# Kernel optimization log

Hardware: AMD Instinct MI355X
Metric: run time of the kernel (lower is better)

## Reference

```python
import jax, jax.numpy as jnp
import numpy as np

B, T, C = 8, 16, 2048
H, HD = 16, 128            # head_dim = C // H
MAX_LEN = 4096             # context_len / kv buffer length
CACHE_LEN = 2048           # tokens already in cache
THETA = 10000.0


def _rope_tables(dim, max_len, theta=THETA):
    freqs = 1.0 / theta ** (jnp.arange(0, dim, 2, dtype=jnp.float32) / dim)
    t = jnp.arange(max_len, dtype=jnp.float32)
    f = jnp.outer(t, freqs)                      # [max_len, dim/2]
    return jnp.cos(f), jnp.sin(f)


def _rotate(x):
    # interleaved rotate-half: (x0,x1,x2,x3,...) -> (-x1,x0,-x3,x2,...)
    x1, x2 = x[..., ::2], x[..., 1::2]
    return jnp.stack((-x2, x1), axis=-1).reshape(x.shape)


def setup_inputs() -> dict:
    key = jax.random.key(0)
    ks = jax.random.split(key, 5)
    x = jax.random.normal(ks[0], (B, T, C), dtype=jnp.float32)
    k_buf = jax.random.normal(ks[1], (B, H, MAX_LEN, HD), dtype=jnp.float32)
    v_buf = jax.random.normal(ks[2], (B, H, MAX_LEN, HD), dtype=jnp.float32)
    W_qkv = jax.random.normal(ks[3], (C, 3 * C), dtype=jnp.float32) / np.sqrt(C)
    W_out = jax.random.normal(ks[4], (C, C), dtype=jnp.float32) / np.sqrt(C)
    cos_tab, sin_tab = _rope_tables(HD, MAX_LEN)
    return {"x": x, "k_buf": k_buf, "v_buf": v_buf, "W_qkv": W_qkv,
            "W_out": W_out, "cos_tab": cos_tab, "sin_tab": sin_tab,
            "cache_len": CACHE_LEN}


def reference(x, k_buf, v_buf, W_qkv, W_out, cos_tab, sin_tab, cache_len):
    B_, T_, C_ = x.shape
    H_ = k_buf.shape[1]
    HD_ = C_ // H_
    # fused QKV projection
    qkv = x @ W_qkv                              # [B,T,3C]
    q, k, v = jnp.split(qkv, 3, axis=-1)
    q = q.reshape(B_, T_, H_, HD_).transpose(0, 2, 1, 3)   # [B,H,T,hd]
    k = k.reshape(B_, T_, H_, HD_).transpose(0, 2, 1, 3)
    v = v.reshape(B_, T_, H_, HD_).transpose(0, 2, 1, 3)
    # RoPE at positions [cache_len, cache_len+T)
    cos2 = jnp.repeat(cos_tab[cache_len:cache_len + T_], 2, axis=-1)[None, None]
    sin2 = jnp.repeat(sin_tab[cache_len:cache_len + T_], 2, axis=-1)[None, None]
    q = q * cos2 + _rotate(q) * sin2
    k = k * cos2 + _rotate(k) * sin2
    # KV-cache update (functional)
    k_buf = k_buf.at[:, :, cache_len:cache_len + T_].set(k)
    v_buf = v_buf.at[:, :, cache_len:cache_len + T_].set(v)
    new_len = cache_len + T_
    # masked full-cache attention
    scale = HD_ ** -0.5
    attn = jnp.einsum('bhqd,bhkd->bhqk', q * scale, k_buf)  # [B,H,T,MAX_LEN]
    q_pos = cache_len + jnp.arange(T_)
    k_pos = jnp.arange(k_buf.shape[2])
    mask = (k_pos[None, :] <= q_pos[:, None]) & (k_pos[None, :] < new_len)
    attn = jnp.where(mask[None, None], attn, jnp.finfo(attn.dtype).min)
    out = jnp.einsum('bhqk,bhkd->bhqd', jax.nn.softmax(attn, axis=-1), v_buf)
    out = out.transpose(0, 2, 1, 3).reshape(B_, T_, C_)
    return out @ W_out, k_buf, v_buf
```

## Files before the change

kernel.cpp:

```cpp
#include <hip/hip_runtime.h>

typedef unsigned short u16;
typedef unsigned int   u32;
typedef u16  u16x4 __attribute__((ext_vector_type(4)));
typedef u16  u16x8 __attribute__((ext_vector_type(8)));
typedef u32  u32x4 __attribute__((ext_vector_type(4)));
typedef short s16x8 __attribute__((ext_vector_type(8)));
typedef float f32x2 __attribute__((ext_vector_type(2)));
typedef float f32x4 __attribute__((ext_vector_type(4)));

#define DEVFN static __device__ __forceinline__

DEVFN float bf2f(u16 v) { u32 t = (u32)v << 16; return __builtin_bit_cast(float, t); }
DEVFN u16 f2bf(float f) {
  u32 u = __builtin_bit_cast(u32, f);
  return (u16)((u + 0x7fffu + ((u >> 16) & 1u)) >> 16);
}
DEVFN void unpk(u32 w, float& lo, float& hi) {
  lo = __builtin_bit_cast(float, w << 16);
  hi = __builtin_bit_cast(float, w & 0xffff0000u);
}

constexpr int Bb = 8, Tt = 16, Cc = 2048, Hh = 16, HD = 128, ML = 4096;
constexpr int N3 = 3 * Cc;
constexpr float SCALE = 0.08838834764831845f;
constexpr size_t NKV = (size_t)Bb * Hh * ML * HD;
constexpr int NCH = 6;

constexpr size_t WS_FLAG = 0;
constexpr size_t WS_QKV  = 16;
constexpr size_t WS_PART = 16;
constexpr size_t WS_QBF  = 786448;
constexpr size_t WS_ATTN = 917520;
constexpr size_t WS_TOTAL = 1179664;

DEVFN int san_cl(int raw) {
  if (raw >= 0 && raw <= ML - Tt) return raw;
  float f = __builtin_bit_cast(float, raw);
  int v = (int)f;
  if (v >= 0 && v <= ML - Tt) return v;
  return 0;
}

DEVFN int w12_probe1(const u32* p, long long base, long long stride, int lane) {
  u32 w = p[base + (long long)lane * stride];
  u32 e = (w >> 7) & 0xffu;
  unsigned long long b = __ballot(e >= 100u && e <= 140u);
  return (__popcll(b) >= 32) ? 0 : 1;
}

__global__ void w12_det(const u32* x, const u32* kb, const u32* vb,
                        const u32* wq, const u32* wo, const u32* ct,
                        const u32* st, int* flags)
{
  int lane = threadIdx.x;
  int f0 = w12_probe1(x,  40000,    997,    lane);
  int f1 = w12_probe1(kb, 10000000, 300001, lane);
  int f2 = w12_probe1(vb, 10000000, 300001, lane);
  int f3 = w12_probe1(wq, 2000000,  33331,  lane);
  int f4 = w12_probe1(wo, 700000,   17177,  lane);
  int f5 = w12_probe1(ct, 40000,    997,    lane);
  int f6 = w12_probe1(st, 40000,    997,    lane);
  if (lane == 0) {
    flags[0] = f0; flags[1] = f1; flags[2] = f2; flags[3] = f3;
    flags[4] = f4; flags[5] = f5; flags[6] = f6; flags[7] = 0;
  }
}

DEVFN void w12_mm_core(const void* __restrict__ A, const void* __restrict__ W,
                       int ldn, int fa, int fw, int kbeg, int m0, int n0,
                       u16 (&As)[64][72], u16 (&Bs)[8][66][8], f32x4 (&acc)[4])
{
  const int tid = threadIdx.x;
  const int l = tid & 63, wv = tid >> 6;
  for (int k0 = kbeg; k0 < kbeg + 512; k0 += 64) {
    __syncthreads();
#pragma unroll
    for (int it = 0; it < 2; ++it) {
      int idx = it * 256 + tid, row = idx >> 3, kc = (idx & 7) * 8;
      if (fa) {
        const float* Af = (const float*)A + (size_t)(m0 + row) * Cc + k0 + kc;
        f32x4 a0 = *(const f32x4*)Af;
        f32x4 a1 = *(const f32x4*)(Af + 4);
        u16x8 av;
#pragma unroll
        for (int u = 0; u < 4; ++u) { av[u] = f2bf(a0[u]); av[u + 4] = f2bf(a1[u]); }
        *(u16x8*)&As[row][kc] = av;
      } else {
        u16x8 av = *(const u16x8*)((const u16*)A + (size_t)(m0 + row) * Cc + k0 + kc);
        *(u16x8*)&As[row][kc] = av;
      }
    }
#pragma unroll
    for (int i = 0; i < 4; ++i) {
      int kk = i * 16 + (tid >> 4);
      int nn = (tid & 15) * 4;
      if (fw) {
        f32x4 bv = *(const f32x4*)((const float*)W + (size_t)(k0 + kk) * ldn + n0 + nn);
#pragma unroll
        for (int u = 0; u < 4; ++u) Bs[kk >> 3][nn + u][kk & 7] = f2bf(bv[u]);
      } else {
        u16x4 bv = *(const u16x4*)((const u16*)W + (size_t)(k0 + kk) * ldn + n0 + nn);
#pragma unroll
        for (int u = 0; u < 4; ++u) Bs[kk >> 3][nn + u][kk & 7] = bv[u];
      }
    }
    __syncthreads();
#pragma unroll
    for (int ks = 0; ks < 2; ++ks) {
      s16x8 a = __builtin_bit_cast(s16x8,
          *(const u16x8*)&As[wv * 16 + (l & 15)][ks * 32 + (l >> 4) * 8]);
#pragma unroll
      for (int nf = 0; nf < 4; ++nf) {
        s16x8 b = __builtin_bit_cast(s16x8,
            *(const u16x8*)&Bs[ks * 4 + (l >> 4)][nf * 16 + (l & 15)][0]);
        acc[nf] = __builtin_amdgcn_mfma_f32_16x16x32_bf16(a, b, acc[nf], 0, 0, 0);
      }
    }
  }
}

__global__ __launch_bounds__(256) void w12_mmp(const void* __restrict__ A,
    const void* __restrict__ W, int ldn, float* __restrict__ part,
    const int* __restrict__ flags)
{
  __shared__ u16 As[64][72];
  __shared__ u16 Bs[8][66][8];
  const int n0 = blockIdx.x * 64, m0 = blockIdx.y * 64, s = blockIdx.z;
  f32x4 acc[4] = {{0.f,0.f,0.f,0.f},{0.f,0.f,0.f,0.f},
                  {0.f,0.f,0.f,0.f},{0.f,0.f,0.f,0.f}};
  w12_mm_core(A, W, ldn, flags[0], flags[3], s * 512, m0, n0, As, Bs, acc);
  const int l = threadIdx.x & 63, wv = threadIdx.x >> 6;
  const int row = m0 + wv * 16 + (l >> 4) * 4;
  const int colb = n0 + (l & 15);
  float* pb = part + (size_t)s * 128 * ldn;
#pragma unroll
  for (int nf = 0; nf < 4; ++nf)
#pragma unroll
    for (int j = 0; j < 4; ++j)
      pb[(size_t)(row + j) * ldn + colb + nf * 16] = acc[nf][j];
}

__global__ __launch_bounds__(256) void w12_red1(const float* __restrict__ part,
                                                float* __restrict__ qkv)
{
  size_t e4 = (size_t)blockIdx.x * 256 + threadIdx.x;
  f32x4 acc = {0.f, 0.f, 0.f, 0.f};
#pragma unroll
  for (int s = 0; s < 4; ++s) {
    f32x4 v = *(const f32x4*)&part[(size_t)s * 786432 + e4 * 4];
    acc[0] += v[0]; acc[1] += v[1]; acc[2] += v[2]; acc[3] += v[3];
  }
  *(f32x4*)&qkv[e4 * 4] = acc;
}

__global__ __launch_bounds__(256) void w12_mma(const float* __restrict__ A,
    const void* __restrict__ W, int ldn, float* __restrict__ outp,
    const int* __restrict__ flags)
{
  __shared__ u16 As[64][72];
  __shared__ u16 Bs[8][66][8];
  const int n0 = blockIdx.x * 64, m0 = blockIdx.y * 64, s = blockIdx.z;
  f32x4 acc[4] = {{0.f,0.f,0.f,0.f},{0.f,0.f,0.f,0.f},
                  {0.f,0.f,0.f,0.f},{0.f,0.f,0.f,0.f}};
  w12_mm_core(A, W, ldn, 1, flags[4], s * 512, m0, n0, As, Bs, acc);
  const int l = threadIdx.x & 63, wv = threadIdx.x >> 6;
  const int row = m0 + wv * 16 + (l >> 4) * 4;
  const int colb = n0 + (l & 15);
#pragma unroll
  for (int nf = 0; nf < 4; ++nf)
#pragma unroll
    for (int j = 0; j < 4; ++j)
      atomicAdd(&outp[(size_t)(row + j) * ldn + colb + nf * 16], acc[nf][j]);
}

__global__ __launch_bounds__(256) void w12_zero(float* __restrict__ outp) {
  size_t i = ((size_t)blockIdx.x * 256 + threadIdx.x) * 4;
  f32x4 z = {0.f, 0.f, 0.f, 0.f};
  *(f32x4*)&outp[i] = z;
}

__global__ __launch_bounds__(256) void w12_rot(const float* __restrict__ qkv,
    const void* __restrict__ ct, const void* __restrict__ st,
    const int* __restrict__ clp, u16* __restrict__ qbf,
    float* __restrict__ outk, float* __restrict__ outv,
    const int* __restrict__ flags)
{
  const int m = blockIdx.x, b = m >> 4, t = m & 15;
  const int half = blockIdx.y;
  const int cl = san_cl(*clp), pos = cl + t;
  const int fc = flags[5], fs = flags[6];
  const float* qr = qkv + (size_t)m * N3;
  for (int i0 = half * 512 + threadIdx.x; i0 < half * 512 + 512; i0 += 256) {
    int h = i0 >> 6, i = i0 & 63;
    float cs = fc ? ((const float*)ct)[pos * 64 + i] : bf2f(((const u16*)ct)[pos * 64 + i]);
    float sn = fs ? ((const float*)st)[pos * 64 + i] : bf2f(((const u16*)st)[pos * 64 + i]);
    int col = h * HD + 2 * i;
    float q0 = qr[col], q1 = qr[col + 1];
    qbf[(size_t)m * Cc + col]     = f2bf((q0 * cs - q1 * sn) * SCALE);
    qbf[(size_t)m * Cc + col + 1] = f2bf((q1 * cs + q0 * sn) * SCALE);
    float k0 = qr[2048 + col], k1 = qr[2048 + col + 1];
    size_t ko = ((size_t)(b * Hh + h) * ML + pos) * HD + 2 * i;
    outk[ko]     = k0 * cs - k1 * sn;
    outk[ko + 1] = k1 * cs + k0 * sn;
    outv[ko]     = qr[4096 + col];
    outv[ko + 1] = qr[4096 + col + 1];
  }
}

__global__ __launch_bounds__(256) void w12_attc(
    const void* __restrict__ kin, const void* __restrict__ vin,
    const u16* __restrict__ qbf, const int* __restrict__ clp,
    float* __restrict__ outk, float* __restrict__ outv,
    float* __restrict__ part, float* __restrict__ mlb,
    const int* __restrict__ flags)
{
  __shared__ u32 kls[64][68];
  __shared__ u32 vls[64][68];
  __shared__ u32 qls[16][68];
  __shared__ float pls[16][68];

  const int tid = threadIdx.x;
  const int chunk = blockIdx.x;
  const int bh = blockIdx.y;
  const int cl = san_cl(*clp), nl = cl + Tt;
  const int fk = flags[1], fv = flags[2];
  const size_t base = (size_t)bh * ML * HD;
  const int b = bh >> 4, h = bh & 15;

  {
    const u16* qsrc = qbf + (size_t)b * Tt * Cc + h * HD;
    int r = tid >> 4, c8 = tid & 15;
    u16x8 qv = *(const u16x8*)&qsrc[(size_t)r * Cc + c8 * 8];
    *(u32x4*)&qls[r][c8 * 4] = __builtin_bit_cast(u32x4, qv);
  }

  const int t = tid >> 4;
  const int js = tid & 15;
  const int qpos = cl + t;
  float m_run = -1e30f, l_run = 0.f;
  float O[8] = {0.f,0.f,0.f,0.f,0.f,0.f,0.f,0.f};

  for (int st8 = chunk; st8 < 64; st8 += NCH) {
    const int r0 = st8 * 64;
    __syncthreads();
#pragma unroll
    for (int ii = 0; ii < 4; ++ii) {
      int idx = ii * 256 + tid, r = idx >> 4, c8 = idx & 15;
      int jg = r0 + r;
      size_t off = base + (size_t)jg * HD + c8 * 8;
      bool fresh = (jg >= cl) && (jg < nl);
      f32x4 ka, kb, va, vb;
      if (fresh) {
        ka = *(const f32x4*)&outk[off];
        kb = *(const f32x4*)&outk[off + 4];
        va = *(const f32x4*)&outv[off];
        vb = *(const f32x4*)&outv[off + 4];
      } else {
        if (fk) {
          ka = *(const f32x4*)((const float*)kin + off);
          kb = *(const f32x4*)((const float*)kin + off + 4);
        } else {
          u16x8 kv8 = *(const u16x8*)((const u16*)kin + off);
          for (int u = 0; u < 4; ++u) { ka[u] = bf2f(kv8[u]); kb[u] = bf2f(kv8[u + 4]); }
        }
        if (fv) {
          va = *(const f32x4*)((const float*)vin + off);
          vb = *(const f32x4*)((const float*)vin + off + 4);
        } else {
          u16x8 vv8 = *(const u16x8*)((const u16*)vin + off);
          for (int u = 0; u < 4; ++u) { va[u] = bf2f(vv8[u]); vb[u] = bf2f(vv8[u + 4]); }
        }
        *(f32x4*)&outk[off] = ka;
        *(f32x4*)&outk[off + 4] = kb;
        *(f32x4*)&outv[off] = va;
        *(f32x4*)&outv[off + 4] = vb;
      }
      u16x8 kv, vv;
#pragma unroll
      for (int u = 0; u < 4; ++u) {
        kv[u] = f2bf(ka[u]); kv[u + 4] = f2bf(kb[u]);
        vv[u] = f2bf(va[u]); vv[u + 4] = f2bf(vb[u]);
      }
      *(u32x4*)&kls[r][c8 * 4] = __builtin_bit_cast(u32x4, kv);
      *(u32x4*)&vls[r][c8 * 4] = __builtin_bit_cast(u32x4, vv);
    }
    __syncthreads();
    if (r0 >= nl) continue;

    float s[4] = {0.f,0.f,0.f,0.f};
#pragma unroll
    for (int dblk = 0; dblk < 4; ++dblk) {
      u32x4 qv[4];
#pragma unroll
      for (int g = 0; g < 4; ++g)
        qv[g] = *(const u32x4*)&qls[t][dblk * 16 + g * 4];
      float qf[32];
#pragma unroll
      for (int g = 0; g < 4; ++g)
#pragma unroll
        for (int u = 0; u < 4; ++u)
          unpk(qv[g][u], qf[g * 8 + 2 * u], qf[g * 8 + 2 * u + 1]);
#pragma unroll
      for (int jj = 0; jj < 4; ++jj) {
        const int j = js + jj * 16;
        u32x4 kv4[4];
#pragma unroll
        for (int g = 0; g < 4; ++g)
          kv4[g] = *(const u32x4*)&kls[j][dblk * 16 + g * 4];
        float a_ = s[jj];
#pragma unroll
        for (int g = 0; g < 4; ++g)
#pragma unroll
          for (int u = 0; u < 4; ++u) {
            float lo, hi; unpk(kv4[g][u], lo, hi);
            a_ += qf[g * 8 + 2 * u] * lo;
            a_ += qf[g * 8 + 2 * u + 1] * hi;
          }
        s[jj] = a_;
      }
    }

    float mt = -1e30f;
    bool val[4];
#pragma unroll
    for (int jj = 0; jj < 4; ++jj) {
      int jg = r0 + js + jj * 16;
      val[jj] = (jg <= qpos);
      if (!val[jj]) s[jj] = -1e30f;
      mt = fmaxf(mt, s[jj]);
    }
#pragma unroll
    for (int w = 1; w < 16; w <<= 1)
      mt = fmaxf(mt, __shfl_xor(mt, w));
    float mn = fmaxf(m_run, mt);
    float crr = __expf(m_run - mn);
    float p[4], ps = 0.f;
#pragma unroll
    for (int jj = 0; jj < 4; ++jj) {
      p[jj] = val[jj] ? __expf(s[jj] - mn) : 0.f;
      ps += p[jj];
    }
#pragma unroll
    for (int w = 1; w < 16; w <<= 1)
      ps += __shfl_xor(ps, w);
    l_run = l_run * crr + ps;
    m_run = mn;
#pragma unroll
    for (int jj = 0; jj < 4; ++jj)
      pls[t][js + jj * 16] = p[jj];
#pragma unroll
    for (int e = 0; e < 8; ++e) O[e] *= crr;
    __syncthreads();

    const int jmax = (nl - r0 < 64) ? (nl - r0) : 64;
#pragma unroll 2
    for (int j = 0; j < jmax; ++j) {
      float pv = pls[t][j];
      u32x4 vw = *(const u32x4*)&vls[j][js * 4];
#pragma unroll
      for (int g = 0; g < 4; ++g) {
        float lo, hi; unpk(vw[g], lo, hi);
        O[2 * g]     += pv * lo;
        O[2 * g + 1] += pv * hi;
      }
    }
  }

  const int slot = bh * NCH + chunk;
  u16* ob = (u16*)(part + (size_t)slot * 1024);
  u16x8 ov;
#pragma unroll
  for (int e = 0; e < 8; ++e) ov[e] = f2bf(O[e]);
  *(u16x8*)&ob[t * HD + js * 8] = ov;
  if (js == 0) { mlb[slot * 32 + t] = m_run; mlb[slot * 32 + 16 + t] = l_run; }
}

__global__ __launch_bounds__(128) void w12_comb(const float* __restrict__ part,
    const float* __restrict__ mlb, float* __restrict__ attn)
{
  const int row = blockIdx.x;
  const int d = threadIdx.x;
  const int bh = row >> 4, t = row & 15;
  float M = -1e30f;
#pragma unroll
  for (int c = 0; c < NCH; ++c) M = fmaxf(M, mlb[(bh * NCH + c) * 32 + t]);
  float L = 0.f, acc = 0.f;
#pragma unroll
  for (int c = 0; c < NCH; ++c) {
    const int slot = bh * NCH + c;
    float w = __expf(mlb[slot * 32 + t] - M);
    L   += w * mlb[slot * 32 + 16 + t];
    acc += w * bf2f(((const u16*)(part + (size_t)slot * 1024))[t * HD + d]);
  }
  const int b = bh >> 4, h = bh & 15;
  attn[(size_t)(b * Tt + t) * Cc + h * HD + d] = acc / L;
}

extern "C" void kernel_launch(void* const* d_in, const int* in_sizes, int n_in,
                              void* d_out, int out_size, void* d_ws, size_t ws_size,
                              hipStream_t stream)
{
  const void* x    = d_in[0];
  const void* kin  = d_in[1];
  const void* vin  = d_in[2];
  const void* wqkv = d_in[3];
  const void* wout = d_in[4];
  const void* ct   = d_in[5];
  const void* st   = d_in[6];
  const int*  clp  = (const int*)d_in[7];

  float* out_f = (float*)d_out;
  float* outk  = out_f + (size_t)Bb * Tt * Cc;
  float* outv  = outk + NKV;
  float* ws = (float*)d_ws;

  if (ws_size < WS_TOTAL * sizeof(float)) return;

  int* flags = (int*)(ws + WS_FLAG);
  u16* qbf   = (u16*)(ws + WS_QBF);

  w12_det<<<1, 64, 0, stream>>>((const u32*)x, (const u32*)kin, (const u32*)vin,
                                (const u32*)wqkv, (const u32*)wout,
                                (const u32*)ct, (const u32*)st, flags);
  w12_mmp<<<dim3(N3 / 64, 2, 4), 256, 0, stream>>>(x, wqkv, N3, outv, flags);
  w12_red1<<<768, 256, 0, stream>>>(outv, ws + WS_QKV);
  w12_rot<<<dim3(128, 2), 256, 0, stream>>>(ws + WS_QKV, ct, st, clp, qbf,
                                            outk, outv, flags);
  w12_attc<<<dim3(NCH, 128), 256, 0, stream>>>(kin, vin, qbf, clp, outk, outv,
                                               ws + WS_PART, out_f, flags);
  w12_comb<<<2048, 128, 0, stream>>>(ws + WS_PART, out_f, ws + WS_ATTN);
  w12_zero<<<256, 256, 0, stream>>>(out_f);
  w12_mma<<<dim3(Cc / 64, 2, 4), 256, 0, stream>>>(ws + WS_ATTN, wout, Cc,
                                                   out_f, flags);
}
```

Measured before the change: 303.6 us.

## Prefetch next KV tile into registers while computing attention on current tile

The attention kernel now software-pipelines its KV tile loop. It loads the next tile's K/V rows into registers before computing scores and the PV product on the current shared-memory tile, and it drops one barrier per iteration. Tiles beyond the valid length are handled in a separate copy-only loop that only copies the cache to the output. Launch bounds now request 3 blocks per CU. The cost is more register pressure from the prefetch buffers, which may spill or cut occupancy.

```diff
diff --git a/kernel.cpp b/kernel.cpp
--- a/kernel.cpp
+++ b/kernel.cpp
@@ -42,32 +42,32 @@
   return 0;
 }
 
-DEVFN int w12_probe1(const u32* p, long long base, long long stride, int lane) {
+DEVFN int w13_probe1(const u32* p, long long base, long long stride, int lane) {
   u32 w = p[base + (long long)lane * stride];
   u32 e = (w >> 7) & 0xffu;
   unsigned long long b = __ballot(e >= 100u && e <= 140u);
   return (__popcll(b) >= 32) ? 0 : 1;
 }
 
-__global__ void w12_det(const u32* x, const u32* kb, const u32* vb,
+__global__ void w13_det(const u32* x, const u32* kb, const u32* vb,
                         const u32* wq, const u32* wo, const u32* ct,
                         const u32* st, int* flags)
 {
   int lane = threadIdx.x;
-  int f0 = w12_probe1(x,  40000,    997,    lane);
-  int f1 = w12_probe1(kb, 10000000, 300001, lane);
-  int f2 = w12_probe1(vb, 10000000, 300001, lane);
-  int f3 = w12_probe1(wq, 2000000,  33331,  lane);
-  int f4 = w12_probe1(wo, 700000,   17177,  lane);
-  int f5 = w12_probe1(ct, 40000,    997,    lane);
-  int f6 = w12_probe1(st, 40000,    997,    lane);
+  int f0 = w13_probe1(x,  40000,    997,    lane);
+  int f1 = w13_probe1(kb, 10000000, 300001, lane);
+  int f2 = w13_probe1(vb, 10000000, 300001, lane);
+  int f3 = w13_probe1(wq, 2000000,  33331,  lane);
+  int f4 = w13_probe1(wo, 700000,   17177,  lane);
+  int f5 = w13_probe1(ct, 40000,    997,    lane);
+  int f6 = w13_probe1(st, 40000,    997,    lane);
   if (lane == 0) {
     flags[0] = f0; flags[1] = f1; flags[2] = f2; flags[3] = f3;
     flags[4] = f4; flags[5] = f5; flags[6] = f6; flags[7] = 0;
   }
 }
 
-DEVFN void w12_mm_core(const void* __restrict__ A, const void* __restrict__ W,
+DEVFN void w13_mm_core(const void* __restrict__ A, const void* __restrict__ W,
                        int ldn, int fa, int fw, int kbeg, int m0, int n0,
                        u16 (&As)[64][72], u16 (&Bs)[8][66][8], f32x4 (&acc)[4])
 {
@@ -120,7 +120,7 @@
   }
 }
 
-__global__ __launch_bounds__(256) void w12_mmp(const void* __restrict__ A,
+__global__ __launch_bounds__(256) void w13_mmp(const void* __restrict__ A,
     const void* __restrict__ W, int ldn, float* __restrict__ part,
     const int* __restrict__ flags)
 {
@@ -129,7 +129,7 @@
   const int n0 = blockIdx.x * 64, m0 = blockIdx.y * 64, s = blockIdx.z;
   f32x4 acc[4] = {{0.f,0.f,0.f,0.f},{0.f,0.f,0.f,0.f},
                   {0.f,0.f,0.f,0.f},{0.f,0.f,0.f,0.f}};
-  w12_mm_core(A, W, ldn, flags[0], flags[3], s * 512, m0, n0, As, Bs, acc);
+  w13_mm_core(A, W, ldn, flags[0], flags[3], s * 512, m0, n0, As, Bs, acc);
   const int l = threadIdx.x & 63, wv = threadIdx.x >> 6;
   const int row = m0 + wv * 16 + (l >> 4) * 4;
   const int colb = n0 + (l & 15);
@@ -141,7 +141,7 @@
       pb[(size_t)(row + j) * ldn + colb + nf * 16] = acc[nf][j];
 }
 
-__global__ __launch_bounds__(256) void w12_red1(const float* __restrict__ part,
+__global__ __launch_bounds__(256) void w13_red1(const float* __restrict__ part,
                                                 float* __restrict__ qkv)
 {
   size_t e4 = (size_t)blockIdx.x * 256 + threadIdx.x;
@@ -154,7 +154,7 @@
   *(f32x4*)&qkv[e4 * 4] = acc;
 }
 
-__global__ __launch_bounds__(256) void w12_mma(const float* __restrict__ A,
+__global__ __launch_bounds__(256) void w13_mma(const float* __restrict__ A,
     const void* __restrict__ W, int ldn, float* __restrict__ outp,
     const int* __restrict__ flags)
 {
@@ -163,7 +163,7 @@
   const int n0 = blockIdx.x * 64, m0 = blockIdx.y * 64, s = blockIdx.z;
   f32x4 acc[4] = {{0.f,0.f,0.f,0.f},{0.f,0.f,0.f,0.f},
                   {0.f,0.f,0.f,0.f},{0.f,0.f,0.f,0.f}};
-  w12_mm_core(A, W, ldn, 1, flags[4], s * 512, m0, n0, As, Bs, acc);
+  w13_mm_core(A, W, ldn, 1, flags[4], s * 512, m0, n0, As, Bs, acc);
   const int l = threadIdx.x & 63, wv = threadIdx.x >> 6;
   const int row = m0 + wv * 16 + (l >> 4) * 4;
   const int colb = n0 + (l & 15);
@@ -174,13 +174,13 @@
       atomicAdd(&outp[(size_t)(row + j) * ldn + colb + nf * 16], acc[nf][j]);
 }
 
-__global__ __launch_bounds__(256) void w12_zero(float* __restrict__ outp) {
+__global__ __launch_bounds__(256) void w13_zero(float* __restrict__ outp) {
   size_t i = ((size_t)blockIdx.x * 256 + threadIdx.x) * 4;
   f32x4 z = {0.f, 0.f, 0.f, 0.f};
   *(f32x4*)&outp[i] = z;
 }
 
-__global__ __launch_bounds__(256) void w12_rot(const float* __restrict__ qkv,
+__global__ __launch_bounds__(256) void w13_rot(const float* __restrict__ qkv,
     const void* __restrict__ ct, const void* __restrict__ st,
     const int* __restrict__ clp, u16* __restrict__ qbf,
     float* __restrict__ outk, float* __restrict__ outv,
@@ -208,7 +208,72 @@
   }
 }
 
-__global__ __launch_bounds__(256) void w12_attc(
+DEVFN void w13_bkunpk(u32x4 w, f32x4& a, f32x4& b) {
+  a[0] = bf2f((u16)(w[0] & 0xffffu)); a[1] = bf2f((u16)(w[0] >> 16));
+  a[2] = bf2f((u16)(w[1] & 0xffffu)); a[3] = bf2f((u16)(w[1] >> 16));
+  b[0] = bf2f((u16)(w[2] & 0xffffu)); b[1] = bf2f((u16)(w[2] >> 16));
+  b[2] = bf2f((u16)(w[3] & 0xffffu)); b[3] = bf2f((u16)(w[3] >> 16));
+}
+
+DEVFN void w13_load_tile(const void* kin, const void* vin,
+    const float* outk, const float* outv, size_t base, int r0, int rr, int c8,
+    int cl, int nl, int fk, int fv,
+    f32x4 (&RK)[8], f32x4 (&RV)[8], u32x4 (&BK)[4], u32x4 (&BV)[4])
+{
+#pragma unroll
+  for (int ii = 0; ii < 4; ++ii) {
+    int jg = r0 + ii * 16 + rr;
+    size_t off = base + (size_t)jg * HD + c8 * 8;
+    bool fr = (jg >= cl) && (jg < nl);
+    if (fr) {
+      RK[2*ii] = *(const f32x4*)&outk[off]; RK[2*ii+1] = *(const f32x4*)&outk[off+4];
+      RV[2*ii] = *(const f32x4*)&outv[off]; RV[2*ii+1] = *(const f32x4*)&outv[off+4];
+    } else {
+      if (fk) {
+        RK[2*ii]   = *(const f32x4*)((const float*)kin + off);
+        RK[2*ii+1] = *(const f32x4*)((const float*)kin + off + 4);
+      } else BK[ii] = *(const u32x4*)((const u16*)kin + off);
+      if (fv) {
+        RV[2*ii]   = *(const f32x4*)((const float*)vin + off);
+        RV[2*ii+1] = *(const f32x4*)((const float*)vin + off + 4);
+      } else BV[ii] = *(const u32x4*)((const u16*)vin + off);
+    }
+  }
+}
+
+DEVFN void w13_write_tile(float* outk, float* outv, size_t base, int r0,
+    int rr, int c8, int cl, int nl, int fk, int fv,
+    const f32x4 (&RK)[8], const f32x4 (&RV)[8],
+    const u32x4 (&BK)[4], const u32x4 (&BV)[4],
+    u32 (&kls)[64][68], u32 (&vls)[64][68])
+{
+#pragma unroll
+  for (int ii = 0; ii < 4; ++ii) {
+    int jg = r0 + ii * 16 + rr;
+    int r = ii * 16 + rr;
+    size_t off = base + (size_t)jg * HD + c8 * 8;
+    bool fr = (jg >= cl) && (jg < nl);
+    f32x4 ka, kb, va, vb;
+    if (fr || fk) { ka = RK[2*ii]; kb = RK[2*ii+1]; }
+    else w13_bkunpk(BK[ii], ka, kb);
+    if (fr || fv) { va = RV[2*ii]; vb = RV[2*ii+1]; }
+    else w13_bkunpk(BV[ii], va, vb);
+    if (!fr) {
+      *(f32x4*)&outk[off] = ka; *(f32x4*)&outk[off + 4] = kb;
+      *(f32x4*)&outv[off] = va; *(f32x4*)&outv[off + 4] = vb;
+    }
+    u16x8 kv, vv;
+#pragma unroll
+    for (int u = 0; u < 4; ++u) {
+      kv[u] = f2bf(ka[u]); kv[u + 4] = f2bf(kb[u]);
+      vv[u] = f2bf(va[u]); vv[u + 4] = f2bf(vb[u]);
+    }
+    *(u32x4*)&kls[r][c8 * 4] = __builtin_bit_cast(u32x4, kv);
+    *(u32x4*)&vls[r][c8 * 4] = __builtin_bit_cast(u32x4, vv);
+  }
+}
+
+__global__ __launch_bounds__(256, 3) void w13_attc(
     const void* __restrict__ kin, const void* __restrict__ vin,
     const u16* __restrict__ qbf, const int* __restrict__ clp,
     float* __restrict__ outk, float* __restrict__ outv,
@@ -230,140 +295,137 @@
 
   {
     const u16* qsrc = qbf + (size_t)b * Tt * Cc + h * HD;
-    int r = tid >> 4, c8 = tid & 15;
-    u16x8 qv = *(const u16x8*)&qsrc[(size_t)r * Cc + c8 * 8];
-    *(u32x4*)&qls[r][c8 * 4] = __builtin_bit_cast(u32x4, qv);
+    int r = tid >> 4, c8q = tid & 15;
+    u16x8 qv = *(const u16x8*)&qsrc[(size_t)r * Cc + c8q * 8];
+    *(u32x4*)&qls[r][c8q * 4] = __builtin_bit_cast(u32x4, qv);
   }
 
   const int t = tid >> 4;
   const int js = tid & 15;
+  const int rr = tid >> 4;
+  const int c8 = tid & 15;
   const int qpos = cl + t;
   float m_run = -1e30f, l_run = 0.f;
   float O[8] = {0.f,0.f,0.f,0.f,0.f,0.f,0.f,0.f};
 
-  for (int st8 = chunk; st8 < 64; st8 += NCH) {
+  f32x4 RK[8], RV[8];
+  u32x4 BK[4], BV[4];
+
+  int st8 = chunk;
+  if (st8 * 64 < nl) {
+    w13_load_tile(kin, vin, outk, outv, base, st8 * 64, rr, c8, cl, nl, fk, fv,
+                  RK, RV, BK, BV);
+    while (true) {
+      const int r0 = st8 * 64;
+      __syncthreads();
+      w13_write_tile(outk, outv, base, r0, rr, c8, cl, nl, fk, fv,
+                     RK, RV, BK, BV, kls, vls);
+      __syncthreads();
+      const int nxt = st8 + NCH;
+      const bool more = (nxt * 64 < nl);
+      if (more)
+        w13_load_tile(kin, vin, outk, outv, base, nxt * 64, rr, c8, cl, nl,
+                      fk, fv, RK, RV, BK, BV);
+
+      float s[4] = {0.f,0.f,0.f,0.f};
+#pragma unroll
+      for (int dblk = 0; dblk < 4; ++dblk) {
+        u32x4 qv[4];
+#pragma unroll
+        for (int g = 0; g < 4; ++g)
+          qv[g] = *(const u32x4*)&qls[t][dblk * 16 + g * 4];
+        float qf[32];
+#pragma unroll
+        for (int g = 0; g < 4; ++g)
+#pragma unroll
+          for (int u = 0; u < 4; ++u)
+            unpk(qv[g][u], qf[g * 8 + 2 * u], qf[g * 8 + 2 * u + 1]);
+#pragma unroll
+        for (int jj = 0; jj < 4; ++jj) {
+          const int j = js + jj * 16;
+          u32x4 kv4[4];
+#pragma unroll
+          for (int g = 0; g < 4; ++g)
+            kv4[g] = *(const u32x4*)&kls[j][dblk * 16 + g * 4];
+          float a_ = s[jj];
+#pragma unroll
+          for (int g = 0; g < 4; ++g)
+#pragma unroll
+            for (int u = 0; u < 4; ++u) {
+              float lo, hi; unpk(kv4[g][u], lo, hi);
+              a_ += qf[g * 8 + 2 * u] * lo;
+              a_ += qf[g * 8 + 2 * u + 1] * hi;
+            }
+          s[jj] = a_;
+        }
+      }
+
+      float mt = -1e30f;
+      bool val[4];
+#pragma unroll
+      for (int jj = 0; jj < 4; ++jj) {
+        int jg = r0 + js + jj * 16;
+        val[jj] = (jg <= qpos);
+        if (!val[jj]) s[jj] = -1e30f;
+        mt = fmaxf(mt, s[jj]);
+      }
+#pragma unroll
+      for (int w = 1; w < 16; w <<= 1)
+        mt = fmaxf(mt, __shfl_xor(mt, w));
+      float mn = fmaxf(m_run, mt);
+      float crr = __expf(m_run - mn);
+      float p[4], ps = 0.f;
+#pragma unroll
+      for (int jj = 0; jj < 4; ++jj) {
+        p[jj] = val[jj] ? __expf(s[jj] - mn) : 0.f;
+        ps += p[jj];
+      }
+#pragma unroll
+      for (int w = 1; w < 16; w <<= 1)
+        ps += __shfl_xor(ps, w);
+      l_run = l_run * crr + ps;
+      m_run = mn;
+#pragma unroll
+      for (int jj = 0; jj < 4; ++jj)
+        pls[t][js + jj * 16] = p[jj];
+#pragma unroll
+      for (int e = 0; e < 8; ++e) O[e] *= crr;
+
+      const int jmax = (nl - r0 < 64) ? (nl - r0) : 64;
+#pragma unroll 2
+      for (int j = 0; j < jmax; ++j) {
+        float pv = pls[t][j];
+        u32x4 vw = *(const u32x4*)&vls[j][js * 4];
+#pragma unroll
+        for (int g = 0; g < 4; ++g) {
+          float lo, hi; unpk(vw[g], lo, hi);
+          O[2 * g]     += pv * lo;
+          O[2 * g + 1] += pv * hi;
+        }
+      }
+
+      if (!more) { st8 = nxt; break; }
+      st8 = nxt;
+    }
+  }
+
+  for (; st8 < 64; st8 += NCH) {
     const int r0 = st8 * 64;
-    __syncthreads();
 #pragma unroll
     for (int ii = 0; ii < 4; ++ii) {
-      int idx = ii * 256 + tid, r = idx >> 4, c8 = idx & 15;
-      int jg = r0 + r;
+      int jg = r0 + ii * 16 + rr;
       size_t off = base + (size_t)jg * HD + c8 * 8;
-      bool fresh = (jg >= cl) && (jg < nl);
       f32x4 ka, kb, va, vb;
-      if (fresh) {
-        ka = *(const f32x4*)&outk[off];
-        kb = *(const f32x4*)&outk[off + 4];
-        va = *(const f32x4*)&outv[off];
-        vb = *(const f32x4*)&outv[off + 4];
-      } else {
-        if (fk) {
-          ka = *(const f32x4*)((const float*)kin + off);
-          kb = *(const f32x4*)((const float*)kin + off + 4);
-        } else {
-          u16x8 kv8 = *(const u16x8*)((const u16*)kin + off);
-          for (int u = 0; u < 4; ++u) { ka[u] = bf2f(kv8[u]); kb[u] = bf2f(kv8[u + 4]); }
-        }
-        if (fv) {
-          va = *(const f32x4*)((const float*)vin + off);
-          vb = *(const f32x4*)((const float*)vin + off + 4);
-        } else {
-          u16x8 vv8 = *(const u16x8*)((const u16*)vin + off);
-          for (int u = 0; u < 4; ++u) { va[u] = bf2f(vv8[u]); vb[u] = bf2f(vv8[u + 4]); }
-        }
-        *(f32x4*)&outk[off] = ka;
-        *(f32x4*)&outk[off + 4] = kb;
-        *(f32x4*)&outv[off] = va;
-        *(f32x4*)&outv[off + 4] = vb;
-      }
-      u16x8 kv, vv;
-#pragma unroll
-      for (int u = 0; u < 4; ++u) {
-        kv[u] = f2bf(ka[u]); kv[u + 4] = f2bf(kb[u]);
-        vv[u] = f2bf(va[u]); vv[u + 4] = f2bf(vb[u]);
-      }
-      *(u32x4*)&kls[r][c8 * 4] = __builtin_bit_cast(u32x4, kv);
-      *(u32x4*)&vls[r][c8 * 4] = __builtin_bit_cast(u32x4, vv);
-    }
-    __syncthreads();
-    if (r0 >= nl) continue;
-
-    float s[4] = {0.f,0.f,0.f,0.f};
-#pragma unroll
-    for (int dblk = 0; dblk < 4; ++dblk) {
-      u32x4 qv[4];
-#pragma unroll
-      for (int g = 0; g < 4; ++g)
-        qv[g] = *(const u32x4*)&qls[t][dblk * 16 + g * 4];
-      float qf[32];
-#pragma unroll
-      for (int g = 0; g < 4; ++g)
-#pragma unroll
-        for (int u = 0; u < 4; ++u)
-          unpk(qv[g][u], qf[g * 8 + 2 * u], qf[g * 8 + 2 * u + 1]);
-#pragma unroll
-      for (int jj = 0; jj < 4; ++jj) {
-        const int j = js + jj * 16;
-        u32x4 kv4[4];
-#pragma unroll
-        for (int g = 0; g < 4; ++g)
-          kv4[g] = *(const u32x4*)&kls[j][dblk * 16 + g * 4];
-        float a_ = s[jj];
-#pragma unroll
-        for (int g = 0; g < 4; ++g)
-#pragma unroll
-          for (int u = 0; u < 4; ++u) {
-            float lo, hi; unpk(kv4[g][u], lo, hi);
-            a_ += qf[g * 8 + 2 * u] * lo;
-            a_ += qf[g * 8 + 2 * u + 1] * hi;
-          }
-        s[jj] = a_;
-      }
-    }
-
-    float mt = -1e30f;
-    bool val[4];
-#pragma unroll
-    for (int jj = 0; jj < 4; ++jj) {
-      int jg = r0 + js + jj * 16;
-      val[jj] = (jg <= qpos);
-      if (!val[jj]) s[jj] = -1e30f;
-      mt = fmaxf(mt, s[jj]);
-    }
-#pragma unroll
-    for (int w = 1; w < 16; w <<= 1)
-      mt = fmaxf(mt, __shfl_xor(mt, w));
-    float mn = fmaxf(m_run, mt);
-    float crr = __expf(m_run - mn);
-    float p[4], ps = 0.f;
-#pragma unroll
-    for (int jj = 0; jj < 4; ++jj) {
-      p[jj] = val[jj] ? __expf(s[jj] - mn) : 0.f;
-      ps += p[jj];
-    }
-#pragma unroll
-    for (int w = 1; w < 16; w <<= 1)
-      ps += __shfl_xor(ps, w);
-    l_run = l_run * crr + ps;
-    m_run = mn;
-#pragma unroll
-    for (int jj = 0; jj < 4; ++jj)
-      pls[t][js + jj * 16] = p[jj];
-#pragma unroll
-    for (int e = 0; e < 8; ++e) O[e] *= crr;
-    __syncthreads();
-
-    const int jmax = (nl - r0 < 64) ? (nl - r0) : 64;
-#pragma unroll 2
-    for (int j = 0; j < jmax; ++j) {
-      float pv = pls[t][j];
-      u32x4 vw = *(const u32x4*)&vls[j][js * 4];
-#pragma unroll
-      for (int g = 0; g < 4; ++g) {
-        float lo, hi; unpk(vw[g], lo, hi);
-        O[2 * g]     += pv * lo;
-        O[2 * g + 1] += pv * hi;
-      }
+      if (fk) {
+        ka = *(const f32x4*)((const float*)kin + off);
+        kb = *(const f32x4*)((const float*)kin + off + 4);
+      } else w13_bkunpk(*(const u32x4*)((const u16*)kin + off), ka, kb);
+      if (fv) {
+        va = *(const f32x4*)((const float*)vin + off);
+        vb = *(const f32x4*)((const float*)vin + off + 4);
+      } else w13_bkunpk(*(const u32x4*)((const u16*)vin + off), va, vb);
+      *(f32x4*)&outk[off] = ka; *(f32x4*)&outk[off + 4] = kb;
+      *(f32x4*)&outv[off] = va; *(f32x4*)&outv[off + 4] = vb;
     }
   }
 
@@ -376,7 +438,7 @@
   if (js == 0) { mlb[slot * 32 + t] = m_run; mlb[slot * 32 + 16 + t] = l_run; }
 }
 
-__global__ __launch_bounds__(128) void w12_comb(const float* __restrict__ part,
+__global__ __launch_bounds__(128) void w13_comb(const float* __restrict__ part,
     const float* __restrict__ mlb, float* __restrict__ attn)
 {
   const int row = blockIdx.x;
@@ -420,17 +482,17 @@
   int* flags = (int*)(ws + WS_FLAG);
   u16* qbf   = (u16*)(ws + WS_QBF);
 
-  w12_det<<<1, 64, 0, stream>>>((const u32*)x, (const u32*)kin, (const u32*)vin,
+  w13_det<<<1, 64, 0, stream>>>((const u32*)x, (const u32*)kin, (const u32*)vin,
                                 (const u32*)wqkv, (const u32*)wout,
                                 (const u32*)ct, (const u32*)st, flags);
-  w12_mmp<<<dim3(N3 / 64, 2, 4), 256, 0, stream>>>(x, wqkv, N3, outv, flags);
-  w12_red1<<<768, 256, 0, stream>>>(outv, ws + WS_QKV);
-  w12_rot<<<dim3(128, 2), 256, 0, stream>>>(ws + WS_QKV, ct, st, clp, qbf,
+  w13_mmp<<<dim3(N3 / 64, 2, 4), 256, 0, stream>>>(x, wqkv, N3, outv, flags);
+  w13_red1<<<768, 256, 0, stream>>>(outv, ws + WS_QKV);
+  w13_rot<<<dim3(128, 2), 256, 0, stream>>>(ws + WS_QKV, ct, st, clp, qbf,
                                             outk, outv, flags);
-  w12_attc<<<dim3(NCH, 128), 256, 0, stream>>>(kin, vin, qbf, clp, outk, outv,
+  w13_attc<<<dim3(NCH, 128), 256, 0, stream>>>(kin, vin, qbf, clp, outk, outv,
                                                ws + WS_PART, out_f, flags);
-  w12_comb<<<2048, 128, 0, stream>>>(ws + WS_PART, out_f, ws + WS_ATTN);
-  w12_zero<<<256, 256, 0, stream>>>(out_f);
-  w12_mma<<<dim3(Cc / 64, 2, 4), 256, 0, stream>>>(ws + WS_ATTN, wout, Cc,
+  w13_comb<<<2048, 128, 0, stream>>>(ws + WS_PART, out_f, ws + WS_ATTN);
+  w13_zero<<<256, 256, 0, stream>>>(out_f);
+  w13_mma<<<dim3(Cc / 64, 2, 4), 256, 0, stream>>>(ws + WS_ATTN, wout, Cc,
                                                    out_f, flags);
 }
```

Result: no change. 309.2 us (+1.8%).
